# Kernel tuning notes

Hardware: AMD Instinct MI355X
Metric: run time of the kernel (lower is better)

The kernel has to match this reference:

```python
import jax, jax.numpy as jnp
from jax import lax
import numpy as np

STRIDES = (2, 2)
PADDING = 'SAME'
EPS = 1e-05


def setup_inputs() -> dict:
    key = jax.random.key(0)
    k1, k2, k3 = jax.random.split(key, 3)
    x = jax.random.normal(k1, (16, 64, 64, 256), dtype=jnp.float32)
    # flax default conv kernel init ~ lecun_normal; plain normal scaled is fine for a math reference
    kernel = jax.random.normal(k2, (4, 4, 256, 128), dtype=jnp.float32) * 0.05
    bias = jax.random.normal(k3, (128,), dtype=jnp.float32) * 0.01
    alpha = jnp.ones((1,), dtype=jnp.float32)
    return {'x': x, 'kernel': kernel, 'bias': bias, 'alpha': alpha}


def reference(x, kernel, bias, alpha):
    # x: [B, H, W, Cin] NHWC; kernel: [kh, kw, Cin, Cout]
    out_features = kernel.shape[-1]

    # main transposed conv: dot-product map  [B, H*2, W*2, Cout]
    dot = lax.conv_transpose(x, kernel, STRIDES, PADDING, transpose_kernel=False)

    # patch squared-sum map: conv_transpose of x**2 with an all-ones kernel
    # of shape kernel_size + (Cin, 1); broadcast over Cout (same math as jnp.repeat)
    ones_k = jnp.ones(kernel.shape[:-1] + (1,), dtype=kernel.dtype)
    patch_sq = lax.conv_transpose(x * x, ones_k, STRIDES, PADDING, transpose_kernel=False)  # [B, H', W', 1]

    # per-filter kernel squared norm, reduced over (kh, kw, Cin) -> [Cout]
    k_sq = jnp.sum(kernel * kernel, axis=(0, 1, 2))

    # ||x_patch - W||^2 = sum(x^2) + sum(W^2) - 2 * <x, W>
    dist_sq = patch_sq + k_sq - 2.0 * dot

    y = (dot * dot) / (dist_sq + EPS)
    y = y + bias  # broadcast over [B, H', W', Cout]

    nf = jnp.float32(out_features)
    scale = (jnp.sqrt(nf) / jnp.log1p(nf)) ** alpha  # alpha shape (1,) broadcasts
    return y * scale
```

## Files before the change

### kernel.cpp

```cpp
#include <hip/hip_runtime.h>
#include <cstdint>
#include <cstddef>

#define CIN   256
#define COUT  128

typedef float  f32x4  __attribute__((ext_vector_type(4)));
typedef __bf16 bf16x8 __attribute__((ext_vector_type(8)));
typedef unsigned int u32x4 __attribute__((ext_vector_type(4)));

#define XPAD_BYTES (16ull*66*66*256*2)
#define WT_OFF     XPAD_BYTES
#define WT_BYTES   (16ull*128*256*2)
#define SPAD_OFF   (WT_OFF + WT_BYTES)
#define SPAD_BYTES (16ull*66*66*4)
#define KSQ_OFF    (SPAD_OFF + SPAD_BYTES)
#define WS_NEEDED  (KSQ_OFF + 512)

__device__ __forceinline__ unsigned short f2bf(float f) {
  unsigned int u = __float_as_uint(f);
  u += 0x7fffu + ((u >> 16) & 1u);
  return (unsigned short)(u >> 16);
}

__device__ __forceinline__ void async16(const void* lds, const void* g) {
  __builtin_amdgcn_global_load_lds(
      (const __attribute__((address_space(1))) unsigned int*)g,
      (__attribute__((address_space(3))) unsigned int*)lds, 16, 0, 0);
}

__global__ __launch_bounds__(256) void prep_x(
    const float* __restrict__ x, unsigned short* __restrict__ xpad,
    float* __restrict__ spad)
{
  int wave = threadIdx.x >> 6, lane = threadIdx.x & 63;
  int p = blockIdx.x * 4 + wave;
  int b = p / 4356;
  int rem = p - b * 4356;
  int iyp = rem / 66, ixp = rem - iyp * 66;
  bool interior = (iyp >= 1 && iyp <= 64 && ixp >= 1 && ixp <= 64);
  f32x4 v = {0.f, 0.f, 0.f, 0.f};
  if (interior) {
    const float* src = x + (((size_t)b*64 + (iyp-1))*64 + (ixp-1))*CIN + lane*4;
    v = *(const f32x4*)src;
  }
  ushort4 h;
  h.x = f2bf(v.x); h.y = f2bf(v.y); h.z = f2bf(v.z); h.w = f2bf(v.w);
  *(ushort4*)(xpad + (size_t)p*CIN + lane*4) = h;
  float s = v.x*v.x + v.y*v.y + v.z*v.z + v.w*v.w;
  #pragma unroll
  for (int off = 32; off > 0; off >>= 1) s += __shfl_down(s, off);
  if (lane == 0) spad[p] = s;
}

__global__ __launch_bounds__(256) void prep_w(
    const float* __restrict__ w, unsigned short* __restrict__ wt,
    float* __restrict__ ksq)
{
  __shared__ __align__(16) unsigned short lw[32*128];
  __shared__ f32x4 red[256];
  int t = threadIdx.x;
  int tap = blockIdx.x >> 3;
  int ci0 = (blockIdx.x & 7) * 32;
  f32x4 sq = {0.f, 0.f, 0.f, 0.f};
  int co4 = (t & 31) * 4;
  #pragma unroll
  for (int i = 0; i < 4; ++i) {
    int ci = (t >> 5) + i*8;
    const float* src = w + ((size_t)(tap*256 + ci0 + ci))*COUT + co4;
    f32x4 v = *(const f32x4*)src;
    sq.x += v.x*v.x; sq.y += v.y*v.y; sq.z += v.z*v.z; sq.w += v.w*v.w;
    ushort4 h; h.x = f2bf(v.x); h.y = f2bf(v.y); h.z = f2bf(v.z); h.w = f2bf(v.w);
    *(ushort4*)&lw[ci*128 + co4] = h;
  }
  red[t] = sq;
  __syncthreads();
  if (t < 32) {
    f32x4 tot = red[t];
    #pragma unroll
    for (int j = 1; j < 8; ++j) {
      f32x4 o = red[t + 32*j];
      tot.x += o.x; tot.y += o.y; tot.z += o.z; tot.w += o.w;
    }
    atomicAdd(ksq + t*4 + 0, tot.x);
    atomicAdd(ksq + t*4 + 1, tot.y);
    atomicAdd(ksq + t*4 + 2, tot.z);
    atomicAdd(ksq + t*4 + 3, tot.w);
  }
  int co = t >> 1, h16 = (t & 1) * 16;
  union { unsigned short u[16]; uint4 q[2]; } tmp;
  #pragma unroll
  for (int i = 0; i < 16; ++i) tmp.u[i] = lw[(h16 + i)*128 + co];
  uint4* dst = (uint4*)(wt + ((size_t)tap*128 + co)*CIN + ci0 + h16);
  dst[0] = tmp.q[0]; dst[1] = tmp.q[1];
}

__global__ __launch_bounds__(512, 1) void yat_main(
    const unsigned short* __restrict__ xpad,
    const unsigned short* __restrict__ wt,
    const float* __restrict__ spad,
    const float* __restrict__ ksq,
    const float* __restrict__ bias,
    const float* __restrict__ alpha,
    float* __restrict__ out)
{
  __shared__ __align__(16) unsigned short xsA[2][23040];
  __shared__ __align__(16) unsigned short xsB[3][8192];
  __shared__ __align__(16) unsigned short scrap[512];
  __shared__ float srow[330];

  int orig = blockIdx.x;
  int bid = (orig & 7) * 128 + (orig >> 3);
  int px = bid & 1, py = (bid >> 1) & 1, u4 = (bid >> 2) & 15, b = bid >> 6;
  int t = threadIdx.x, wave = t >> 6, lane = t & 63;
  int rp = wave & 3, coh = wave >> 2;
  int l15 = lane & 15, l4 = lane >> 4;
  int bRow0 = u4*4 + py;

  if (t < 330) {
    int r = t / 66, c = t - r*66;
    srow[t] = spad[((size_t)b*66 + bRow0 + r)*66 + c];
  }
  asm volatile("s_waitcnt vmcnt(0) lgkmcnt(0)" ::: "memory");
  __syncthreads();

  const char* srcA[6];
  unsigned short* dstA[6];
  int mulA[6];
  #pragma unroll
  for (int r = 0; r < 6; ++r) {
    int k = r*8 + wave;
    int kk = (k < 45) ? k : 44;
    int row = kk / 9, cb = kk - row*9;
    int col = cb*8 + (lane >> 3); if (col > 65) col = 65;
    int qs = (lane & 7) ^ (col & 7);
    srcA[r] = (const char*)xpad
            + (((size_t)(b*66 + bRow0 + row))*66 + col)*512 + qs*16;
    dstA[r] = (k < 45) ? (&xsA[0][0] + row*4608 + cb*512) : &scrap[0];
    mulA[r] = (k < 45) ? 23040 : 0;
  }
  const char* srcB[2][4];
  unsigned short* dstB[2];
  #pragma unroll
  for (int r = 0; r < 2; ++r) {
    int k = r*8 + wave;
    int co = k*8 + (lane >> 3);
    int qs = (lane & 7) ^ (co & 7);
    dstB[r] = &xsB[0][0] + k*512;
    #pragma unroll
    for (int ab = 0; ab < 4; ++ab) {
      int tap = (py + 2*(ab >> 1))*4 + px + 2*(ab & 1);
      srcB[r][ab] = (const char*)wt + (size_t)tap*65536 + (size_t)co*512 + qs*16;
    }
  }

  unsigned aB0 = (unsigned)(unsigned long long)(&xsA[0][0]) + (unsigned)(rp*9216);
  unsigned abA[2][2];
  #pragma unroll
  for (int bb = 0; bb < 2; ++bb) {
    int c7 = (l15 + px + bb) & 7;
    #pragma unroll
    for (int sub = 0; sub < 2; ++sub)
      abA[bb][sub] = aB0 + (l15 + px + bb)*128 + (((sub*4 + l4) ^ c7) << 4);
  }
  unsigned bB0 = (unsigned)(unsigned long long)(&xsB[0][0]) + (coh*64 + l15)*128;
  unsigned abB[2];
  #pragma unroll
  for (int sub = 0; sub < 2; ++sub)
    abB[sub] = bB0 + (((sub*4 + l4) ^ (l15 & 7)) << 4);

  f32x4 acc[4][4];
  #pragma unroll
  for (int i = 0; i < 4; ++i)
    #pragma unroll
    for (int j = 0; j < 4; ++j)
      acc[i][j] = (f32x4){0.f, 0.f, 0.f, 0.f};

#define SB  __builtin_amdgcn_sched_barrier(0)
#define BAR __builtin_amdgcn_s_barrier()
#define VMW(N) do { asm volatile("s_waitcnt vmcnt(" #N ")" ::: "memory"); SB; } while (0)
#define LGKW(N) do { asm volatile("s_waitcnt lgkmcnt(" #N ")" ::: "memory"); SB; } while (0)
#define DSR(dst, addr, off)                                                \
  asm volatile("ds_read_b128 %0, %1 offset:%c2"                            \
               : "=v"(dst) : "v"(addr), "i"(off))

#define STAGE_A(BUF, S) {                                                  \
    async16(dstA[0] + (BUF)*mulA[0], srcA[0] + (S)*128);                   \
    async16(dstA[1] + (BUF)*mulA[1], srcA[1] + (S)*128);                   \
    async16(dstA[2] + (BUF)*mulA[2], srcA[2] + (S)*128);                   \
    async16(dstA[3] + (BUF)*mulA[3], srcA[3] + (S)*128);                   \
    async16(dstA[4] + (BUF)*mulA[4], srcA[4] + (S)*128);                   \
    async16(dstA[5] + (BUF)*mulA[5], srcA[5] + (S)*128); }

#define STAGE_B(TT, BI) {                                                  \
    async16(dstB[0] + (BI)*8192, srcB[0][(TT)&3] + ((TT)>>2)*128);         \
    async16(dstB[1] + (BI)*8192, srcB[1][(TT)&3] + ((TT)>>2)*128); }

#define MFMA16(A_, B_)                                                     \
  { _Pragma("unroll")                                                      \
    for (int mt = 0; mt < 4; ++mt)                                         \
      _Pragma("unroll")                                                    \
      for (int nt = 0; nt < 4; ++nt)                                       \
        acc[mt][nt] = __builtin_amdgcn_mfma_f32_16x16x32_bf16(             \
            __builtin_bit_cast(bf16x8, A_[mt]),                            \
            __builtin_bit_cast(bf16x8, B_[nt]),                            \
            acc[mt][nt], 0, 0, 0); }

#define COMPUTE(BUFA, AA, BB, BI) {                                        \
    u32x4 Af0[4], Bf0[4], Af1[4], Bf1[4];                                  \
    DSR(Af0[0], abA[BB][0], (BUFA)*46080 + (AA)*9216 + 0);                 \
    DSR(Af0[1], abA[BB][0], (BUFA)*46080 + (AA)*9216 + 2048);              \
    DSR(Af0[2], abA[BB][0], (BUFA)*46080 + (AA)*9216 + 4096);              \
    DSR(Af0[3], abA[BB][0], (BUFA)*46080 + (AA)*9216 + 6144);              \
    DSR(Bf0[0], abB[0], (BI)*16384 + 0);                                   \
    DSR(Bf0[1], abB[0], (BI)*16384 + 2048);                                \
    DSR(Bf0[2], abB[0], (BI)*16384 + 4096);                                \
    DSR(Bf0[3], abB[0], (BI)*16384 + 6144);                                \
    DSR(Af1[0], abA[BB][1], (BUFA)*46080 + (AA)*9216 + 0);                 \
    DSR(Af1[1], abA[BB][1], (BUFA)*46080 + (AA)*9216 + 2048);              \
    DSR(Af1[2], abA[BB][1], (BUFA)*46080 + (AA)*9216 + 4096);              \
    DSR(Af1[3], abA[BB][1], (BUFA)*46080 + (AA)*9216 + 6144);              \
    DSR(Bf1[0], abB[1], (BI)*16384 + 0);                                   \
    DSR(Bf1[1], abB[1], (BI)*16384 + 2048);                                \
    DSR(Bf1[2], abB[1], (BI)*16384 + 4096);                                \
    DSR(Bf1[3], abB[1], (BI)*16384 + 6144);                                \
    LGKW(8);                                                               \
    __builtin_amdgcn_s_setprio(1); MFMA16(Af0, Bf0);                       \
    __builtin_amdgcn_s_setprio(0);                                         \
    LGKW(0);                                                               \
    __builtin_amdgcn_s_setprio(1); MFMA16(Af1, Bf1);                       \
    __builtin_amdgcn_s_setprio(0); SB; }

  SB;
  STAGE_B(0, 0);
  STAGE_A(0, 0);
  STAGE_B(1, 1);
  SB;
  VMW(2); BAR; STAGE_B(2, 2);  STAGE_A(1, 1); SB; COMPUTE(0, 0, 0, 0);
  VMW(8); BAR; STAGE_B(3, 0);  SB;               COMPUTE(0, 0, 1, 1);
  VMW(8); BAR; STAGE_B(4, 1);  SB;               COMPUTE(0, 1, 0, 2);
  VMW(2); BAR; STAGE_B(5, 2);  SB;               COMPUTE(0, 1, 1, 0);
  VMW(2); BAR; STAGE_B(6, 0);  STAGE_A(0, 2); SB; COMPUTE(1, 0, 0, 1);
  VMW(8); BAR; STAGE_B(7, 1);  SB;               COMPUTE(1, 0, 1, 2);
  VMW(8); BAR; STAGE_B(8, 2);  SB;               COMPUTE(1, 1, 0, 0);
  VMW(2); BAR; STAGE_B(9, 0);  SB;               COMPUTE(1, 1, 1, 1);
  VMW(2); BAR; STAGE_B(10, 1); STAGE_A(1, 3); SB; COMPUTE(0, 0, 0, 2);
  VMW(8); BAR; STAGE_B(11, 2); SB;               COMPUTE(0, 0, 1, 0);
  VMW(8); BAR; STAGE_B(12, 0); SB;               COMPUTE(0, 1, 0, 1);
  VMW(2); BAR; STAGE_B(13, 1); SB;               COMPUTE(0, 1, 1, 2);
  VMW(2); BAR; STAGE_B(14, 2); SB;               COMPUTE(1, 0, 0, 0);
  VMW(2); BAR; STAGE_B(15, 0); SB;               COMPUTE(1, 0, 1, 1);
  VMW(2); BAR;                                   COMPUTE(1, 1, 0, 2);
  VMW(0); BAR;                                   COMPUTE(1, 1, 1, 0);

#undef SB
#undef BAR
#undef VMW
#undef LGKW
#undef DSR
#undef STAGE_A
#undef STAGE_B
#undef MFMA16
#undef COMPUTE

  float scale = powf(sqrtf(128.f) / log1pf(128.f), alpha[0]);
  float kq[4], bi[4];
  #pragma unroll
  for (int nt = 0; nt < 4; ++nt) {
    int n = coh*64 + nt*16 + l15;
    kq[nt] = ksq[n]; bi[nt] = bias[n];
  }
  int oy = 2*(u4*4 + rp) + py;
  size_t orow = ((size_t)b*128 + oy) * 128 * COUT;
  #pragma unroll
  for (int mt = 0; mt < 4; ++mt) {
    #pragma unroll
    for (int r = 0; r < 4; ++r) {
      int v = mt*16 + l4*4 + r;
      int vpx = v + px;
      float ps = srow[rp*66 + vpx] + srow[rp*66 + vpx + 1]
               + srow[rp*66 + 66 + vpx] + srow[rp*66 + 66 + vpx + 1];
      #pragma unroll
      for (int nt = 0; nt < 4; ++nt) {
        float dot = acc[mt][nt][r];
        float dist = ps + kq[nt] - 2.f*dot + 1e-5f;
        float y = (dot*dot/dist + bi[nt]) * scale;
        int n = coh*64 + nt*16 + l15;
        out[orow + (size_t)(2*v + px)*COUT + n] = y;
      }
    }
  }
}

__global__ __launch_bounds__(256) void fb_ksq(const float* __restrict__ w,
                                              float* __restrict__ ksq) {
  __shared__ float red[256];
  int co = blockIdx.x, t = threadIdx.x;
  float s = 0.f;
  for (int j = t; j < 4096; j += 256) { float v = w[(size_t)j*COUT + co]; s += v*v; }
  red[t] = s; __syncthreads();
  for (int off = 128; off > 0; off >>= 1) {
    if (t < off) red[t] += red[t + off];
    __syncthreads();
  }
  if (t == 0) ksq[co] = red[0];
}

__global__ __launch_bounds__(256) void fb_main(
    const float* __restrict__ x, const float* __restrict__ w,
    const float* __restrict__ bias, const float* __restrict__ alpha,
    const float* __restrict__ ksq, float* __restrict__ out)
{
  size_t idx = (size_t)blockIdx.x * 256 + threadIdx.x;
  int co = (int)(idx & 127);
  int ox = (int)((idx >> 7) & 127);
  int oy = (int)((idx >> 14) & 127);
  int b  = (int)(idx >> 21);
  int py = oy & 1, px = ox & 1, u = oy >> 1, v = ox >> 1;
  float dot = 0.f, ps = 0.f;
  for (int a = 0; a < 2; ++a) {
    int iy = u + py + a - 1;
    if (iy < 0 || iy > 63) continue;
    for (int b2 = 0; b2 < 2; ++b2) {
      int ix = v + px + b2 - 1;
      if (ix < 0 || ix > 63) continue;
      const float* xp = x + (((size_t)b*64 + iy)*64 + ix)*CIN;
      const float* wp = w + ((size_t)((py + 2*a)*4 + (px + 2*b2))*CIN)*COUT + co;
      for (int ci = 0; ci < CIN; ++ci) {
        float xv = xp[ci];
        dot += xv * wp[(size_t)ci*COUT];
        ps  += xv * xv;
      }
    }
  }
  float dist = ps + ksq[co] - 2.f*dot + 1e-5f;
  float scale = powf(sqrtf(128.f) / log1pf(128.f), alpha[0]);
  out[idx] = (dot*dot/dist + bias[co]) * scale;
}

extern "C" void kernel_launch(void* const* d_in, const int* in_sizes, int n_in,
                              void* d_out, int out_size, void* d_ws, size_t ws_size,
                              hipStream_t stream)
{
  const float* x     = (const float*)d_in[0];
  const float* w     = (const float*)d_in[1];
  const float* bias  = (const float*)d_in[2];
  const float* alpha = (const float*)d_in[3];
  float* out = (float*)d_out;

  if (ws_size < WS_NEEDED) {
    float* ksq = (float*)d_ws;
    fb_ksq<<<128, 256, 0, stream>>>(w, ksq);
    fb_main<<<131072, 256, 0, stream>>>(x, w, bias, alpha, ksq, out);
    return;
  }

  unsigned short* xpad = (unsigned short*)d_ws;
  unsigned short* wtp  = (unsigned short*)((char*)d_ws + WT_OFF);
  float* spad = (float*)((char*)d_ws + SPAD_OFF);
  float* ksq  = (float*)((char*)d_ws + KSQ_OFF);

  hipMemsetAsync(ksq, 0, 512, stream);
  prep_x<<<17424, 256, 0, stream>>>(x, xpad, spad);
  prep_w<<<128, 256, 0, stream>>>(w, wtp, ksq);
  yat_main<<<1024, 512, 0, stream>>>(xpad, wtp, spad, ksq, bias, alpha, out);
}
```

Measured before the change: 117.4 us.

## Software-pipeline LDS fragment reads across MFMA phases with ping-pong registers

Restructures the unrolled main loop so the LDS reads for the next half-step go into a second register set (Xa/Xb, Ya/Yb) while MFMAs run on the previous set. The loads for the following stage are issued before the barrier, so ds_read latency overlaps matrix math instead of stalling at each stage start. B staging is also issued one stage earlier (three B buffers in flight at the prologue). This adds register pressure and reorders the barrier and waitcnt points, which risks lower occupancy or a hazard on buffer reuse.

```diff
diff --git a/kernel.cpp b/kernel.cpp
--- a/kernel.cpp
+++ b/kernel.cpp
@@ -176,10 +176,12 @@
     for (int j = 0; j < 4; ++j)
       acc[i][j] = (f32x4){0.f, 0.f, 0.f, 0.f};
 
+  u32x4 Xa[4], Xb[4], Ya[4], Yb[4];
+
 #define SB  __builtin_amdgcn_sched_barrier(0)
 #define BAR __builtin_amdgcn_s_barrier()
 #define VMW(N) do { asm volatile("s_waitcnt vmcnt(" #N ")" ::: "memory"); SB; } while (0)
-#define LGKW(N) do { asm volatile("s_waitcnt lgkmcnt(" #N ")" ::: "memory"); SB; } while (0)
+#define LGK(N) do { asm volatile("s_waitcnt lgkmcnt(" #N ")" ::: "memory"); SB; } while (0)
 #define DSR(dst, addr, off)                                                \
   asm volatile("ds_read_b128 %0, %1 offset:%c2"                            \
                : "=v"(dst) : "v"(addr), "i"(off))
@@ -195,6 +197,16 @@
 #define STAGE_B(TT, BI) {                                                  \
     async16(dstB[0] + (BI)*8192, srcB[0][(TT)&3] + ((TT)>>2)*128);         \
     async16(dstB[1] + (BI)*8192, srcB[1][(TT)&3] + ((TT)>>2)*128); }
+
+#define READS(RA, RB_, BUFA, AA, BB, SUB, BI) {                            \
+    DSR(RA[0], abA[BB][SUB], (BUFA)*46080 + (AA)*9216 + 0);                \
+    DSR(RA[1], abA[BB][SUB], (BUFA)*46080 + (AA)*9216 + 2048);             \
+    DSR(RA[2], abA[BB][SUB], (BUFA)*46080 + (AA)*9216 + 4096);             \
+    DSR(RA[3], abA[BB][SUB], (BUFA)*46080 + (AA)*9216 + 6144);             \
+    DSR(RB_[0], abB[SUB], (BI)*16384 + 0);                                 \
+    DSR(RB_[1], abB[SUB], (BI)*16384 + 2048);                              \
+    DSR(RB_[2], abB[SUB], (BI)*16384 + 4096);                              \
+    DSR(RB_[3], abB[SUB], (BI)*16384 + 6144); }
 
 #define MFMA16(A_, B_)                                                     \
   { _Pragma("unroll")                                                      \
@@ -206,62 +218,124 @@
             __builtin_bit_cast(bf16x8, B_[nt]),                            \
             acc[mt][nt], 0, 0, 0); }
 
-#define COMPUTE(BUFA, AA, BB, BI) {                                        \
-    u32x4 Af0[4], Bf0[4], Af1[4], Bf1[4];                                  \
-    DSR(Af0[0], abA[BB][0], (BUFA)*46080 + (AA)*9216 + 0);                 \
-    DSR(Af0[1], abA[BB][0], (BUFA)*46080 + (AA)*9216 + 2048);              \
-    DSR(Af0[2], abA[BB][0], (BUFA)*46080 + (AA)*9216 + 4096);              \
-    DSR(Af0[3], abA[BB][0], (BUFA)*46080 + (AA)*9216 + 6144);              \
-    DSR(Bf0[0], abB[0], (BI)*16384 + 0);                                   \
-    DSR(Bf0[1], abB[0], (BI)*16384 + 2048);                                \
-    DSR(Bf0[2], abB[0], (BI)*16384 + 4096);                                \
-    DSR(Bf0[3], abB[0], (BI)*16384 + 6144);                                \
-    DSR(Af1[0], abA[BB][1], (BUFA)*46080 + (AA)*9216 + 0);                 \
-    DSR(Af1[1], abA[BB][1], (BUFA)*46080 + (AA)*9216 + 2048);              \
-    DSR(Af1[2], abA[BB][1], (BUFA)*46080 + (AA)*9216 + 4096);              \
-    DSR(Af1[3], abA[BB][1], (BUFA)*46080 + (AA)*9216 + 6144);              \
-    DSR(Bf1[0], abB[1], (BI)*16384 + 0);                                   \
-    DSR(Bf1[1], abB[1], (BI)*16384 + 2048);                                \
-    DSR(Bf1[2], abB[1], (BI)*16384 + 4096);                                \
-    DSR(Bf1[3], abB[1], (BI)*16384 + 6144);                                \
-    LGKW(8);                                                               \
-    __builtin_amdgcn_s_setprio(1); MFMA16(Af0, Bf0);                       \
-    __builtin_amdgcn_s_setprio(0);                                         \
-    LGKW(0);                                                               \
-    __builtin_amdgcn_s_setprio(1); MFMA16(Af1, Bf1);                       \
-    __builtin_amdgcn_s_setprio(0); SB; }
+#define PHB(A_, B_) { LGK(8); __builtin_amdgcn_s_setprio(1); MFMA16(A_, B_); \
+                      __builtin_amdgcn_s_setprio(0); SB; }
+#define PHF(A_, B_) { __builtin_amdgcn_s_setprio(1); MFMA16(A_, B_);       \
+                      __builtin_amdgcn_s_setprio(0); SB; }
 
   SB;
   STAGE_B(0, 0);
   STAGE_A(0, 0);
   STAGE_B(1, 1);
+  STAGE_B(2, 2);
   SB;
-  VMW(2); BAR; STAGE_B(2, 2);  STAGE_A(1, 1); SB; COMPUTE(0, 0, 0, 0);
-  VMW(8); BAR; STAGE_B(3, 0);  SB;               COMPUTE(0, 0, 1, 1);
-  VMW(8); BAR; STAGE_B(4, 1);  SB;               COMPUTE(0, 1, 0, 2);
-  VMW(2); BAR; STAGE_B(5, 2);  SB;               COMPUTE(0, 1, 1, 0);
-  VMW(2); BAR; STAGE_B(6, 0);  STAGE_A(0, 2); SB; COMPUTE(1, 0, 0, 1);
-  VMW(8); BAR; STAGE_B(7, 1);  SB;               COMPUTE(1, 0, 1, 2);
-  VMW(8); BAR; STAGE_B(8, 2);  SB;               COMPUTE(1, 1, 0, 0);
-  VMW(2); BAR; STAGE_B(9, 0);  SB;               COMPUTE(1, 1, 1, 1);
-  VMW(2); BAR; STAGE_B(10, 1); STAGE_A(1, 3); SB; COMPUTE(0, 0, 0, 2);
-  VMW(8); BAR; STAGE_B(11, 2); SB;               COMPUTE(0, 0, 1, 0);
-  VMW(8); BAR; STAGE_B(12, 0); SB;               COMPUTE(0, 1, 0, 1);
-  VMW(2); BAR; STAGE_B(13, 1); SB;               COMPUTE(0, 1, 1, 2);
-  VMW(2); BAR; STAGE_B(14, 2); SB;               COMPUTE(1, 0, 0, 0);
-  VMW(2); BAR; STAGE_B(15, 0); SB;               COMPUTE(1, 0, 1, 1);
-  VMW(2); BAR;                                   COMPUTE(1, 1, 0, 2);
-  VMW(0); BAR;                                   COMPUTE(1, 1, 1, 0);
+  VMW(4); BAR; SB;
+  READS(Xa, Xb, 0,0,0, 0, 0); SB;
+
+  READS(Ya, Yb, 0,0,0, 1, 0); SB;
+  PHB(Xa, Xb);
+  LGK(0); VMW(2); BAR; SB;
+  STAGE_B(3, 0); STAGE_A(1, 1); SB;
+  READS(Xa, Xb, 0,0,1, 0, 1); SB;
+  PHF(Ya, Yb);
+  READS(Ya, Yb, 0,0,1, 1, 1); SB;
+  PHB(Xa, Xb);
+  LGK(0); VMW(8); BAR; SB;
+  STAGE_B(4, 1); SB;
+  READS(Xa, Xb, 0,1,0, 0, 2); SB;
+  PHF(Ya, Yb);
+  READS(Ya, Yb, 0,1,0, 1, 2); SB;
+  PHB(Xa, Xb);
+  LGK(0); VMW(2); BAR; SB;
+  STAGE_B(5, 2); SB;
+  READS(Xa, Xb, 0,1,1, 0, 0); SB;
+  PHF(Ya, Yb);
+  READS(Ya, Yb, 0,1,1, 1, 0); SB;
+  PHB(Xa, Xb);
+  LGK(0); VMW(2); BAR; SB;
+  STAGE_B(6, 0); SB;
+  READS(Xa, Xb, 1,0,0, 0, 1); SB;
+  PHF(Ya, Yb);
+  READS(Ya, Yb, 1,0,0, 1, 1); SB;
+  PHB(Xa, Xb);
+  LGK(0); VMW(2); BAR; SB;
+  STAGE_B(7, 1); STAGE_A(0, 2); SB;
+  READS(Xa, Xb, 1,0,1, 0, 2); SB;
+  PHF(Ya, Yb);
+  READS(Ya, Yb, 1,0,1, 1, 2); SB;
+  PHB(Xa, Xb);
+  LGK(0); VMW(8); BAR; SB;
+  STAGE_B(8, 2); SB;
+  READS(Xa, Xb, 1,1,0, 0, 0); SB;
+  PHF(Ya, Yb);
+  READS(Ya, Yb, 1,1,0, 1, 0); SB;
+  PHB(Xa, Xb);
+  LGK(0); VMW(2); BAR; SB;
+  STAGE_B(9, 0); SB;
+  READS(Xa, Xb, 1,1,1, 0, 1); SB;
+  PHF(Ya, Yb);
+  READS(Ya, Yb, 1,1,1, 1, 1); SB;
+  PHB(Xa, Xb);
+  LGK(0); VMW(2); BAR; SB;
+  STAGE_B(10, 1); SB;
+  READS(Xa, Xb, 0,0,0, 0, 2); SB;
+  PHF(Ya, Yb);
+  READS(Ya, Yb, 0,0,0, 1, 2); SB;
+  PHB(Xa, Xb);
+  LGK(0); VMW(2); BAR; SB;
+  STAGE_B(11, 2); STAGE_A(1, 3); SB;
+  READS(Xa, Xb, 0,0,1, 0, 0); SB;
+  PHF(Ya, Yb);
+  READS(Ya, Yb, 0,0,1, 1, 0); SB;
+  PHB(Xa, Xb);
+  LGK(0); VMW(8); BAR; SB;
+  STAGE_B(12, 0); SB;
+  READS(Xa, Xb, 0,1,0, 0, 1); SB;
+  PHF(Ya, Yb);
+  READS(Ya, Yb, 0,1,0, 1, 1); SB;
+  PHB(Xa, Xb);
+  LGK(0); VMW(2); BAR; SB;
+  STAGE_B(13, 1); SB;
+  READS(Xa, Xb, 0,1,1, 0, 2); SB;
+  PHF(Ya, Yb);
+  READS(Ya, Yb, 0,1,1, 1, 2); SB;
+  PHB(Xa, Xb);
+  LGK(0); VMW(2); BAR; SB;
+  STAGE_B(14, 2); SB;
+  READS(Xa, Xb, 1,0,0, 0, 0); SB;
+  PHF(Ya, Yb);
+  READS(Ya, Yb, 1,0,0, 1, 0); SB;
+  PHB(Xa, Xb);
+  LGK(0); VMW(2); BAR; SB;
+  STAGE_B(15, 0); SB;
+  READS(Xa, Xb, 1,0,1, 0, 1); SB;
+  PHF(Ya, Yb);
+  READS(Ya, Yb, 1,0,1, 1, 1); SB;
+  PHB(Xa, Xb);
+  LGK(0); VMW(2); BAR; SB;
+  READS(Xa, Xb, 1,1,0, 0, 2); SB;
+  PHF(Ya, Yb);
+  READS(Ya, Yb, 1,1,0, 1, 2); SB;
+  PHB(Xa, Xb);
+  LGK(0); VMW(0); BAR; SB;
+  READS(Xa, Xb, 1,1,1, 0, 0); SB;
+  PHF(Ya, Yb);
+  READS(Ya, Yb, 1,1,1, 1, 0); SB;
+  PHB(Xa, Xb);
+  LGK(0);
+  PHF(Ya, Yb);
 
 #undef SB
 #undef BAR
 #undef VMW
-#undef LGKW
+#undef LGK
 #undef DSR
 #undef STAGE_A
 #undef STAGE_B
+#undef READS
 #undef MFMA16
-#undef COMPUTE
+#undef PHB
+#undef PHF
 
   float scale = powf(sqrtf(128.f) / log1pf(128.f), alpha[0]);
   float kq[4], bi[4];
```

Measured after the change: 117.4 us. Within noise of the previous version (-0.0%).
